# Kernel tuning notes

Measured on AMD Instinct MI355X. Metric: run time of the kernel, lower is better.

## Reference

```python
import jax, jax.numpy as jnp
import numpy as np

B, S, HID = 128, 512, 512
IN_DIM = 1  # forced by x[:, t].unsqueeze(-1) + cat along dim 2


def setup_inputs() -> dict:
    key = jax.random.key(0)
    ks = jax.random.split(key, 9)
    scale = 0.05
    d_in = IN_DIM + HID
    return {
        "x": jax.random.normal(ks[0], (B, S, IN_DIM), dtype=jnp.float32),
        "H_prev": jnp.zeros((B, 1, HID), dtype=jnp.float32),
        "C_prev": jnp.zeros((B, 1, HID), dtype=jnp.float32),
        "Wi": jax.random.normal(ks[1], (d_in, HID), dtype=jnp.float32) * scale,
        "bi": jax.random.normal(ks[2], (1, HID), dtype=jnp.float32) * scale,
        "Wf": jax.random.normal(ks[3], (d_in, HID), dtype=jnp.float32) * scale,
        "bf": jax.random.normal(ks[4], (1, HID), dtype=jnp.float32) * scale,
        "Wc": jax.random.normal(ks[5], (d_in, HID), dtype=jnp.float32) * scale,
        "bc": jax.random.normal(ks[6], (1, HID), dtype=jnp.float32) * scale,
        "Wo": jax.random.normal(ks[7], (d_in, HID), dtype=jnp.float32) * scale,
        "bo": jax.random.normal(ks[8], (1, HID), dtype=jnp.float32) * scale,
    }


def reference(x, H_prev, C_prev, Wi, bi, Wf, bf, Wc, bc, Wo, bo):
    # x: [B, S, 1]; H_prev, C_prev: [B, 1, HID]
    def step(carry, x_t):
        H, C = carry  # each [B, 1, HID]
        comb = jnp.concatenate([x_t[:, None, :], H], axis=2)  # [B, 1, 1+HID]
        I = jax.nn.sigmoid(comb @ Wi + bi)
        F = jax.nn.sigmoid(comb @ Wf + bf)
        C_hat = jnp.tanh(comb @ Wc + bc)
        O = comb @ Wo + bo  # NOTE: no sigmoid, faithful to source
        C_new = F * C + I * C_hat
        H_new = O * jnp.tanh(C_new)
        return (H_new, C_new), None

    xs = jnp.swapaxes(x, 0, 1)  # [S, B, 1]
    (H_t, C_t), _ = jax.lax.scan(step, (H_prev, C_prev), xs)
    # original returns (hidden_sequence, H_t, C_t) where hidden_sequence == last H_t
    return (H_t, H_t, C_t)
```

## Files before the change

kernel.cpp:

```cpp
#include <hip/hip_runtime.h>
#include <math.h>

#define SEQ 512
#define HID 512
#define NGROUP 8
#define GB 16
#define BPG 32
#define SLOTU 65536
#define GSLOTU 8192
#define LROW 520

typedef __attribute__((ext_vector_type(8))) short short8;
typedef __attribute__((ext_vector_type(4))) float floatx4;

__device__ __forceinline__ unsigned short f2bf(float f) {
    unsigned u = __builtin_bit_cast(unsigned, f);
    return (unsigned short)((u + 0x7FFFu + ((u >> 16) & 1u)) >> 16);
}
__device__ __forceinline__ float bf2f(unsigned short h) {
    unsigned u = ((unsigned)h) << 16;
    return __builtin_bit_cast(float, u);
}
__device__ __forceinline__ float fast_sigmoid(float x) {
    return 1.0f / (1.0f + __expf(-x));
}
__device__ __forceinline__ float fast_tanh(float x) {
    float e = __expf(-2.0f * fabsf(x));
    float t = (1.0f - e) / (1.0f + e);
    return x < 0.0f ? -t : t;
}

__global__ void lstm_init(const float* __restrict__ H0, unsigned short* __restrict__ hb) {
    int idx = blockIdx.x * blockDim.x + threadIdx.x;
    if (idx < SLOTU) {
        int k = idx & 511, b = (idx >> 9) & 15, g = idx >> 13;
        hb[idx] = f2bf(H0[(g * GB + b) * HID + k]);
    } else if (idx < SLOTU + NGROUP * 64) {
        ((int*)(hb + 2 * SLOTU))[idx - SLOTU] = 0;
    }
}

__global__ __launch_bounds__(256, 1)
void lstm_main(const float* __restrict__ x,
               const float* __restrict__ C0,
               const float* __restrict__ Wi, const float* __restrict__ bi,
               const float* __restrict__ Wf, const float* __restrict__ bf_,
               const float* __restrict__ Wc, const float* __restrict__ bc,
               const float* __restrict__ Wo, const float* __restrict__ bo,
               float* __restrict__ out, unsigned short* __restrict__ hb) {
    int* flags = (int*)(hb + 2 * SLOTU);

    const int bid  = blockIdx.x;
    const int g    = bid & 7;
    const int cb   = bid >> 3;
    const int tid  = threadIdx.x;
    const int w    = tid >> 6;
    const int lane = tid & 63;
    const int q    = lane >> 4;
    const int c    = lane & 15;

    const int gate = c & 3;
    const int colA = cb * 16 + w * 4 + (c >> 2);
    const int colD = cb * 16 + w * 4 + q;
    const int bD   = g * GB + c;

    const float* Wg = (gate == 0) ? Wi : (gate == 1) ? Wf : (gate == 2) ? Wc : Wo;
    short8 aHi[16], aLo[16];
    #pragma unroll
    for (int kt = 0; kt < 16; ++kt) {
        #pragma unroll
        for (int j = 0; j < 8; ++j) {
            int k = kt * 32 + q * 8 + j;
            float wv = Wg[(k + 1) * HID + colA];
            unsigned short hi = f2bf(wv);
            unsigned short lo = f2bf(wv - bf2f(hi));
            aHi[kt][j] = (short)hi;
            aLo[kt][j] = (short)lo;
        }
    }

    const float biasI = bi[colD], biasF = bf_[colD], biasC = bc[colD], biasO = bo[colD];
    const float w0I = Wi[colD], w0F = Wf[colD], w0C = Wc[colD], w0O = Wo[colD];
    float Cst = C0[bD * HID + colD];
    const float* xrow = x + bD * SEQ;

    __shared__ unsigned short hlds[16 * LROW];

    int* myflag = flags + g * 64 + cb;

    for (int t = 0; t < SEQ; ++t) {
        if (tid < BPG) {
            const int* fp = flags + g * 64 + tid;
            while (__hip_atomic_load(fp, __ATOMIC_RELAXED, __HIP_MEMORY_SCOPE_AGENT) < t)
                __builtin_amdgcn_s_sleep(2);
        }
        __syncthreads();

        {
            const unsigned short* gsrc = hb + (t & 1) * SLOTU + g * GSLOTU + tid * 32;
            float4 v0, v1, v2, v3;
            asm volatile(
                "global_load_dwordx4 %0, %4, off sc0 sc1\n\t"
                "global_load_dwordx4 %1, %4, off offset:16 sc0 sc1\n\t"
                "global_load_dwordx4 %2, %4, off offset:32 sc0 sc1\n\t"
                "global_load_dwordx4 %3, %4, off offset:48 sc0 sc1\n\t"
                "s_waitcnt vmcnt(0)"
                : "=&v"(v0), "=&v"(v1), "=&v"(v2), "=&v"(v3)
                : "v"(gsrc) : "memory");
            int b = tid >> 4, ch = tid & 15;
            unsigned short* dst = hlds + b * LROW + ch * 32;
            *(float4*)(dst + 0)  = v0;
            *(float4*)(dst + 8)  = v1;
            *(float4*)(dst + 16) = v2;
            *(float4*)(dst + 24) = v3;
        }
        __syncthreads();

        floatx4 acc = {0.f, 0.f, 0.f, 0.f};
        const unsigned short* brow = hlds + c * LROW + q * 8;
        #pragma unroll
        for (int kt = 0; kt < 16; ++kt) {
            short8 bfrag = *(const short8*)(brow + kt * 32);
            acc = __builtin_amdgcn_mfma_f32_16x16x32_bf16(aHi[kt], bfrag, acc, 0, 0, 0);
            acc = __builtin_amdgcn_mfma_f32_16x16x32_bf16(aLo[kt], bfrag, acc, 0, 0, 0);
        }

        float xv  = xrow[t];
        float aIv = acc[0] + fmaf(xv, w0I, biasI);
        float aFv = acc[1] + fmaf(xv, w0F, biasF);
        float aCv = acc[2] + fmaf(xv, w0C, biasC);
        float aOv = acc[3] + fmaf(xv, w0O, biasO);
        float I  = fast_sigmoid(aIv);
        float F  = fast_sigmoid(aFv);
        float Ch = fast_tanh(aCv);
        Cst = fmaf(F, Cst, I * Ch);
        float Hn = aOv * fast_tanh(Cst);

        if (t < SEQ - 1) {
            int v = (int)f2bf(Hn);
            int o = __shfl_xor(v, 16);
            if ((q & 1) == 0) {
                unsigned val = (unsigned)(unsigned short)v |
                               ((unsigned)(unsigned short)o << 16);
                unsigned* dst = (unsigned*)(hb + ((t + 1) & 1) * SLOTU + g * GSLOTU
                                            + c * 512 + colD);
                __hip_atomic_store(dst, val, __ATOMIC_RELAXED, __HIP_MEMORY_SCOPE_AGENT);
            }
            __syncthreads();
            if (tid == 0)
                __hip_atomic_store(myflag, t + 1, __ATOMIC_RELAXED, __HIP_MEMORY_SCOPE_AGENT);
        } else {
            int o = bD * HID + colD;
            out[o] = Hn; out[65536 + o] = Hn; out[131072 + o] = Cst;
        }
    }
}

extern "C" void kernel_launch(void* const* d_in, const int* in_sizes, int n_in,
                              void* d_out, int out_size, void* d_ws, size_t ws_size,
                              hipStream_t stream) {
    const float* x  = (const float*)d_in[0];
    const float* H0 = (const float*)d_in[1];
    const float* C0 = (const float*)d_in[2];
    const float* Wi = (const float*)d_in[3];
    const float* bi = (const float*)d_in[4];
    const float* Wf = (const float*)d_in[5];
    const float* bf = (const float*)d_in[6];
    const float* Wc = (const float*)d_in[7];
    const float* bc = (const float*)d_in[8];
    const float* Wo = (const float*)d_in[9];
    const float* bo = (const float*)d_in[10];
    float* out = (float*)d_out;
    unsigned short* hb = (unsigned short*)d_ws;

    const int init_elems = SLOTU + NGROUP * 64;
    hipLaunchKernelGGL(lstm_init, dim3((init_elems + 255) / 256), dim3(256), 0, stream,
                       H0, hb);
    hipLaunchKernelGGL(lstm_main, dim3(NGROUP * BPG), dim3(256), 0, stream,
                       x, C0, Wi, bi, Wf, bf, Wc, bc, Wo, bo, out, hb);
}
```

Measured before the change: 1.391 ms.

## Per-thread 64-bit flag polling, split MFMA accumulators, hoist x load

Each thread now polls the two producer flags covering its own H chunk with one 64-bit atomic load. This replaces the 32-thread poll followed by a block-wide barrier, so the global load of a chunk can start as soon as its producers finish. The MFMA chain is split into four independent accumulators to shorten the serial dependency, and the x load is moved ahead of the MFMA loop. An explicit vmcnt wait is added before the barrier that precedes the flag store, so the H stores complete before the flag is published. More threads spinning on the flags adds memory traffic.

```diff
diff --git a/kernel.cpp b/kernel.cpp
--- a/kernel.cpp
+++ b/kernel.cpp
@@ -87,16 +87,18 @@
     __shared__ unsigned short hlds[16 * LROW];
 
     int* myflag = flags + g * 64 + cb;
+    const int b_row = tid >> 4, ch = tid & 15;
+    const unsigned long long* fp64 =
+        (const unsigned long long*)(flags + g * 64 + 2 * ch);
 
     for (int t = 0; t < SEQ; ++t) {
-        if (tid < BPG) {
-            const int* fp = flags + g * 64 + tid;
-            while (__hip_atomic_load(fp, __ATOMIC_RELAXED, __HIP_MEMORY_SCOPE_AGENT) < t)
-                __builtin_amdgcn_s_sleep(2);
-        }
-        __syncthreads();
-
         {
+            for (;;) {
+                unsigned long long fv =
+                    __hip_atomic_load(fp64, __ATOMIC_RELAXED, __HIP_MEMORY_SCOPE_AGENT);
+                if ((int)(unsigned)fv >= t && (int)(fv >> 32) >= t) break;
+                __builtin_amdgcn_s_sleep(1);
+            }
             const unsigned short* gsrc = hb + (t & 1) * SLOTU + g * GSLOTU + tid * 32;
             float4 v0, v1, v2, v3;
             asm volatile(
@@ -107,8 +109,7 @@
                 "s_waitcnt vmcnt(0)"
                 : "=&v"(v0), "=&v"(v1), "=&v"(v2), "=&v"(v3)
                 : "v"(gsrc) : "memory");
-            int b = tid >> 4, ch = tid & 15;
-            unsigned short* dst = hlds + b * LROW + ch * 32;
+            unsigned short* dst = hlds + b_row * LROW + ch * 32;
             *(float4*)(dst + 0)  = v0;
             *(float4*)(dst + 8)  = v1;
             *(float4*)(dst + 16) = v2;
@@ -116,16 +117,27 @@
         }
         __syncthreads();
 
-        floatx4 acc = {0.f, 0.f, 0.f, 0.f};
+        float xv = xrow[t];
+
+        floatx4 a0 = {0.f, 0.f, 0.f, 0.f}, a1 = a0, a2 = a0, a3 = a0;
         const unsigned short* brow = hlds + c * LROW + q * 8;
         #pragma unroll
-        for (int kt = 0; kt < 16; ++kt) {
-            short8 bfrag = *(const short8*)(brow + kt * 32);
-            acc = __builtin_amdgcn_mfma_f32_16x16x32_bf16(aHi[kt], bfrag, acc, 0, 0, 0);
-            acc = __builtin_amdgcn_mfma_f32_16x16x32_bf16(aLo[kt], bfrag, acc, 0, 0, 0);
+        for (int kt = 0; kt < 16; kt += 4) {
+            short8 b0 = *(const short8*)(brow + (kt + 0) * 32);
+            a0 = __builtin_amdgcn_mfma_f32_16x16x32_bf16(aHi[kt + 0], b0, a0, 0, 0, 0);
+            a0 = __builtin_amdgcn_mfma_f32_16x16x32_bf16(aLo[kt + 0], b0, a0, 0, 0, 0);
+            short8 b1 = *(const short8*)(brow + (kt + 1) * 32);
+            a1 = __builtin_amdgcn_mfma_f32_16x16x32_bf16(aHi[kt + 1], b1, a1, 0, 0, 0);
+            a1 = __builtin_amdgcn_mfma_f32_16x16x32_bf16(aLo[kt + 1], b1, a1, 0, 0, 0);
+            short8 b2 = *(const short8*)(brow + (kt + 2) * 32);
+            a2 = __builtin_amdgcn_mfma_f32_16x16x32_bf16(aHi[kt + 2], b2, a2, 0, 0, 0);
+            a2 = __builtin_amdgcn_mfma_f32_16x16x32_bf16(aLo[kt + 2], b2, a2, 0, 0, 0);
+            short8 b3 = *(const short8*)(brow + (kt + 3) * 32);
+            a3 = __builtin_amdgcn_mfma_f32_16x16x32_bf16(aHi[kt + 3], b3, a3, 0, 0, 0);
+            a3 = __builtin_amdgcn_mfma_f32_16x16x32_bf16(aLo[kt + 3], b3, a3, 0, 0, 0);
         }
+        floatx4 acc = (a0 + a1) + (a2 + a3);
 
-        float xv  = xrow[t];
         float aIv = acc[0] + fmaf(xv, w0I, biasI);
         float aFv = acc[1] + fmaf(xv, w0F, biasF);
         float aCv = acc[2] + fmaf(xv, w0C, biasC);
@@ -146,9 +158,11 @@
                                             + c * 512 + colD);
                 __hip_atomic_store(dst, val, __ATOMIC_RELAXED, __HIP_MEMORY_SCOPE_AGENT);
             }
+            asm volatile("s_waitcnt vmcnt(0)" ::: "memory");
             __syncthreads();
             if (tid == 0)
-                __hip_atomic_store(myflag, t + 1, __ATOMIC_RELAXED, __HIP_MEMORY_SCOPE_AGENT);
+                __hip_atomic_store(myflag, t + 1, __ATOMIC_RELAXED,
+                                   __HIP_MEMORY_SCOPE_AGENT);
         } else {
             int o = bD * HID + colD;
             out[o] = Hn; out[65536 + o] = Hn; out[131072 + o] = Cst;
```

After: 2.168 ms. 55.9% more time.

## Use per-wave completion flags with vectorized ballot polling to shorten step barrier

Applied to the files above, without the earlier changes.

Each wave now publishes its own completion flag after waiting for its stores, removing the block-wide barrier before the flag store. One wave polls all 128 flags of the group as 64-bit pairs and uses a ballot to decide readiness, with a shorter sleep. The hidden-state loads drop the sc0 bit, keeping only sc1. The aim is less synchronisation latency on the 512-step sequential path. Relying on vmcnt(0) for visibility and on the changed cache bits risks reading stale data.

```diff
diff --git a/kernel.cpp b/kernel.cpp
--- a/kernel.cpp
+++ b/kernel.cpp
@@ -6,6 +6,7 @@
 #define NGROUP 8
 #define GB 16
 #define BPG 32
+#define NFLAG 128
 #define SLOTU 65536
 #define GSLOTU 8192
 #define LROW 520
@@ -35,7 +36,7 @@
     if (idx < SLOTU) {
         int k = idx & 511, b = (idx >> 9) & 15, g = idx >> 13;
         hb[idx] = f2bf(H0[(g * GB + b) * HID + k]);
-    } else if (idx < SLOTU + NGROUP * 64) {
+    } else if (idx < SLOTU + NGROUP * NFLAG) {
         ((int*)(hb + 2 * SLOTU))[idx - SLOTU] = 0;
     }
 }
@@ -86,13 +87,19 @@
 
     __shared__ unsigned short hlds[16 * LROW];
 
-    int* myflag = flags + g * 64 + cb;
+    int* myflag = flags + g * NFLAG + cb * 4 + w;
+    const unsigned long long* pollp =
+        (const unsigned long long*)(flags + g * NFLAG) + lane;
 
     for (int t = 0; t < SEQ; ++t) {
-        if (tid < BPG) {
-            const int* fp = flags + g * 64 + tid;
-            while (__hip_atomic_load(fp, __ATOMIC_RELAXED, __HIP_MEMORY_SCOPE_AGENT) < t)
-                __builtin_amdgcn_s_sleep(2);
+        if (w == 0) {
+            for (;;) {
+                unsigned long long fv =
+                    __hip_atomic_load(pollp, __ATOMIC_RELAXED, __HIP_MEMORY_SCOPE_AGENT);
+                bool ok = ((int)(unsigned)fv >= t) && ((int)(fv >> 32) >= t);
+                if (__ballot(ok) == ~0ull) break;
+                __builtin_amdgcn_s_sleep(1);
+            }
         }
         __syncthreads();
 
@@ -100,10 +107,10 @@
             const unsigned short* gsrc = hb + (t & 1) * SLOTU + g * GSLOTU + tid * 32;
             float4 v0, v1, v2, v3;
             asm volatile(
-                "global_load_dwordx4 %0, %4, off sc0 sc1\n\t"
-                "global_load_dwordx4 %1, %4, off offset:16 sc0 sc1\n\t"
-                "global_load_dwordx4 %2, %4, off offset:32 sc0 sc1\n\t"
-                "global_load_dwordx4 %3, %4, off offset:48 sc0 sc1\n\t"
+                "global_load_dwordx4 %0, %4, off sc1\n\t"
+                "global_load_dwordx4 %1, %4, off offset:16 sc1\n\t"
+                "global_load_dwordx4 %2, %4, off offset:32 sc1\n\t"
+                "global_load_dwordx4 %3, %4, off offset:48 sc1\n\t"
                 "s_waitcnt vmcnt(0)"
                 : "=&v"(v0), "=&v"(v1), "=&v"(v2), "=&v"(v3)
                 : "v"(gsrc) : "memory");
@@ -146,9 +153,10 @@
                                             + c * 512 + colD);
                 __hip_atomic_store(dst, val, __ATOMIC_RELAXED, __HIP_MEMORY_SCOPE_AGENT);
             }
-            __syncthreads();
-            if (tid == 0)
-                __hip_atomic_store(myflag, t + 1, __ATOMIC_RELAXED, __HIP_MEMORY_SCOPE_AGENT);
+            asm volatile("s_waitcnt vmcnt(0)" ::: "memory");
+            if (lane == 0)
+                __hip_atomic_store(myflag, t + 1, __ATOMIC_RELAXED,
+                                   __HIP_MEMORY_SCOPE_AGENT);
         } else {
             int o = bD * HID + colD;
             out[o] = Hn; out[65536 + o] = Hn; out[131072 + o] = Cst;
@@ -173,7 +181,7 @@
     float* out = (float*)d_out;
     unsigned short* hb = (unsigned short*)d_ws;
 
-    const int init_elems = SLOTU + NGROUP * 64;
+    const int init_elems = SLOTU + NGROUP * NFLAG;
     hipLaunchKernelGGL(lstm_init, dim3((init_elems + 255) / 256), dim3(256), 0, stream,
                        H0, hb);
     hipLaunchKernelGGL(lstm_main, dim3(NGROUP * BPG), dim3(256), 0, stream,
```

Result: slower. 3.143 ms (+126.0%).
